# Kernel tuning notes

Hardware: AMD Instinct MI355X
Metric: run time of the kernel (lower is better)

The kernel has to match this reference:

```python
import jax, jax.numpy as jnp
import numpy as np

RESO = 32          # triplane/voxel resolution
VIT = 16           # ViT patch grid resolution
PAD = 0.1
C_TRI = 64         # triplane channels per plane
C_IMG = 1280       # image feature channels
C_IN = 128         # inner (attention) channels
C_OUT = 64
NH = 8
HD = C_IN // NH
IMG_SIZE = 224.0


def pos_enc(d_model, length):
    pos = jnp.arange(length, dtype=jnp.float32)[:, None]
    div = jnp.exp(jnp.arange(0, d_model, 2, dtype=jnp.float32) * (-np.log(10000.0) / d_model))
    pe = jnp.zeros((length, d_model), jnp.float32)
    pe = pe.at[:, 0::2].set(jnp.sin(pos * div))
    pe = pe.at[:, 1::2].set(jnp.cos(pos * div))
    return pe


def bilinear_sample(feats, gx, gy):
    # feats: [B, J, H, W, C]; gx, gy: [B, J, N] in [-1, 1]; align_corners=True
    B, J, Hh, Ww, _ = feats.shape
    ux = (gx + 1.0) * 0.5 * (Ww - 1)
    uy = (gy + 1.0) * 0.5 * (Hh - 1)
    x0 = jnp.floor(ux).astype(jnp.int32)
    y0 = jnp.floor(uy).astype(jnp.int32)
    wx = (ux - x0)[..., None]
    wy = (uy - y0)[..., None]
    x1 = jnp.clip(x0 + 1, 0, Ww - 1)
    y1 = jnp.clip(y0 + 1, 0, Hh - 1)
    x0 = jnp.clip(x0, 0, Ww - 1)
    y0 = jnp.clip(y0, 0, Hh - 1)
    bi = jnp.arange(B)[:, None, None]
    ji = jnp.arange(J)[None, :, None]
    f00 = feats[bi, ji, y0, x0]
    f01 = feats[bi, ji, y0, x1]
    f10 = feats[bi, ji, y1, x0]
    f11 = feats[bi, ji, y1, x1]
    return (f00 * (1 - wx) * (1 - wy) + f01 * wx * (1 - wy)
            + f10 * (1 - wx) * wy + f11 * wx * wy)


def forward(triplane_feat, image_feat, proj_mat, k_w, k_b, q_w, q_b, v_w, v_b,
            in_w, in_b, out_w, out_b, proj_w, proj_b):
    B, n_img = image_feat.shape[0], image_feat.shape[1]
    N = RESO ** 3
    img = image_feat[:, :, 1:, :]                        # drop CLS -> [B,J,256,C_IMG]
    image_pe = pos_enc(C_IN, VIT * VIT)[None, None]      # [1,1,256,C_IN]
    k_feat = img @ k_w.T + k_b + image_pe
    v_feat = img @ v_w.T + v_b + image_pe
    k_map = k_feat.reshape(B, n_img, VIT, VIT, C_IN)     # [B,J,H,W,C]
    v_map = v_feat.reshape(B, n_img, VIT, VIT, C_IN)

    # voxel coords -> project into each camera
    idx = jnp.arange(RESO)
    X, Y, Z = jnp.meshgrid(idx, idx, idx, indexing='ij')
    vox = jnp.stack([X, Y, Z], -1).reshape(N, 3).astype(jnp.float32)
    vox = (vox / (RESO - 1) - 0.5) * 2.0 * (1.0 + PAD + 1e-5)
    homo = jnp.concatenate([vox, jnp.ones((N, 1), jnp.float32)], -1)  # [N,4]
    pc = jnp.einsum('nk,bjik->bjni', homo, proj_mat)                   # [B,J,N,4]
    px = pc[..., 0] / pc[..., 2]
    py = pc[..., 1] / pc[..., 2]
    gx = jnp.clip((px / (IMG_SIZE - 1) - 0.5) * 2.0, -1.0, 1.0)
    gy = jnp.clip((py / (IMG_SIZE - 1) - 0.5) * 2.0, -1.0, 1.0)
    # The torch code does a 3D grid_sample whose depth coordinate lands exactly
    # on each image index (align_corners=True), so it reduces to per-image
    # bilinear sampling on the 16x16 token maps.
    k_s = bilinear_sample(k_map, gx, gy)   # [B,J,N,C_IN]
    v_s = bilinear_sample(v_map, gx, gy)

    # triplane features expanded to the voxel grid (voxel order n = x*R^2+y*R+z)
    xz, xy, yz = jnp.split(triplane_feat, 3, axis=2)     # each [B,C,R,R]
    xz_t = jnp.transpose(xz, (0, 3, 2, 1))               # [B,x,z,C]
    xy_t = jnp.transpose(xy, (0, 3, 2, 1))               # [B,x,y,C]
    yz_t = jnp.transpose(yz, (0, 3, 2, 1))               # [B,y,z,C]
    shp = (B, RESO, RESO, RESO, C_TRI)
    xz_v = jnp.broadcast_to(xz_t[:, :, None, :, :], shp)
    xy_v = jnp.broadcast_to(xy_t[:, :, :, None, :], shp)
    yz_v = jnp.broadcast_to(yz_t[:, None, :, :, :], shp)
    tri = jnp.concatenate([xz_v, xy_v, yz_v], -1).reshape(B, N, 3 * C_TRI)
    q = tri @ q_w.T + q_b + pos_enc(C_IN, N)[None]       # [B,N,C_IN]

    # per-voxel cross attention (q_len=1, kv_len=n_img); torch MHA semantics
    Wq, Wk, Wv = in_w[:C_IN], in_w[C_IN:2 * C_IN], in_w[2 * C_IN:]
    bq, bk, bv = in_b[:C_IN], in_b[C_IN:2 * C_IN], in_b[2 * C_IN:]
    qh = (q @ Wq.T + bq).reshape(B, N, NH, HD)
    k_t = jnp.transpose(k_s, (0, 2, 1, 3))               # [B,N,J,C]
    v_t = jnp.transpose(v_s, (0, 2, 1, 3))
    kh = (k_t @ Wk.T + bk).reshape(B, N, n_img, NH, HD)
    vh = (v_t @ Wv.T + bv).reshape(B, N, n_img, NH, HD)
    logits = jnp.einsum('bnhd,bnjhd->bnhj', qh, kh) / np.sqrt(HD).astype(np.float32)
    attn = jax.nn.softmax(logits, axis=-1)
    o = jnp.einsum('bnhj,bnjhd->bnhd', attn, vh).reshape(B, N, C_IN)
    o = o @ out_w.T + out_b

    # mean-pool volume back to three planes
    vol = o.reshape(B, RESO, RESO, RESO, C_IN)             # [b,x,y,z,c]
    xz_o = jnp.transpose(vol.mean(axis=2), (0, 2, 1, 3))   # [b,z,x,c]
    xy_o = jnp.transpose(vol.mean(axis=3), (0, 2, 1, 3))   # [b,y,x,c]
    yz_o = jnp.transpose(vol.mean(axis=1), (0, 2, 1, 3))   # [b,z,y,c]
    planes = jnp.concatenate([xz_o, xy_o, yz_o], axis=1)   # [B,3R,R,C_IN]
    out = planes @ proj_w.T + proj_b
    return jnp.transpose(out, (0, 3, 1, 2))                # [B,C_OUT,3R,R]


def setup_inputs() -> dict:
    key = jax.random.key(0)
    ks = jax.random.split(key, 10)
    B, J = 2, 5
    s = 0.02
    base = jnp.array([[200., 0., 112., 0.],
                      [0., 200., 112., 0.],
                      [0., 0., 1., 3.5],
                      [0., 0., 0., 1.]], jnp.float32)
    return {
        'triplane_feat': jax.random.normal(ks[0], (B, C_TRI, 3 * RESO, RESO), jnp.float32),
        'image_feat': jax.random.normal(ks[1], (B, J, VIT * VIT + 1, C_IMG), jnp.float32),
        'proj_mat': base[None, None] + 0.01 * jax.random.normal(ks[2], (B, J, 4, 4), jnp.float32),
        'valid_frames': jnp.ones((B, J), jnp.int32),
        'k_w': s * jax.random.normal(ks[3], (C_IN, C_IMG), jnp.float32), 'k_b': jnp.zeros((C_IN,), jnp.float32),
        'q_w': s * jax.random.normal(ks[4], (C_IN, 3 * C_TRI), jnp.float32), 'q_b': jnp.zeros((C_IN,), jnp.float32),
        'v_w': s * jax.random.normal(ks[5], (C_IN, C_IMG), jnp.float32), 'v_b': jnp.zeros((C_IN,), jnp.float32),
        'in_w': s * jax.random.normal(ks[6], (3 * C_IN, C_IN), jnp.float32), 'in_b': jnp.zeros((3 * C_IN,), jnp.float32),
        'out_w': s * jax.random.normal(ks[7], (C_IN, C_IN), jnp.float32), 'out_b': jnp.zeros((C_IN,), jnp.float32),
        'proj_w': s * jax.random.normal(ks[8], (C_OUT, C_IN), jnp.float32), 'proj_b': jnp.zeros((C_OUT,), jnp.float32),
    }


def reference(triplane_feat, image_feat, proj_mat, valid_frames, k_w, k_b, q_w, q_b,
              v_w, v_b, in_w, in_b, out_w, out_b, proj_w, proj_b):
    # valid_frames matches the torch forward signature but is unused in its body
    return forward(triplane_feat, image_feat, proj_mat, k_w, k_b, q_w, q_b,
                   v_w, v_b, in_w, in_b, out_w, out_b, proj_w, proj_b)
```

## Files before the change

### kernel.cpp

```cpp
#include <hip/hip_runtime.h>
#include <hip/hip_bf16.h>
#include <cstddef>

#define NVOX 32768
#define J5 5
#define KB2 1472
typedef __hip_bfloat16 bf16;
typedef __attribute__((ext_vector_type(8))) short bf16x8v;
typedef __attribute__((ext_vector_type(4))) float f32x4;

static __device__ __forceinline__ float pe_val(int pos, int c) {
  float dv = expf((float)(c & ~1) * (-0.0719557841560639f));
  float arg = (float)pos * dv;
  return (c & 1) ? cosf(arg) : sinf(arg);
}
static __device__ __forceinline__ short f2b(float f) {
  __hip_bfloat16 h = __float2bfloat16(f);
  return *reinterpret_cast<short*>(&h);
}
static __device__ __forceinline__ float b2f(short s) {
  __hip_bfloat16 h = *reinterpret_cast<__hip_bfloat16*>(&s);
  return __bfloat162float(h);
}
static __device__ __forceinline__ float2 cmul(float2 a, float2 b) {
  return make_float2(a.x * b.x - a.y * b.y, a.x * b.y + a.y * b.x);
}

#define NB_TABS   24
#define NB_WQPE   64
#define NB_WQC    96
#define NB_WO     32
#define NB_QCB    1
#define NB_TRI    1536
#define NB_FOLDW  1280
#define NB_PETAB  128
#define NB_WIN    128
#define NB_CB     1
#define B_TABS   0
#define B_WQPE   (B_TABS + NB_TABS)
#define B_WQC    (B_WQPE + NB_WQPE)
#define B_WO     (B_WQC + NB_WQC)
#define B_QCB    (B_WO + NB_WO)
#define B_TRI    (B_QCB + NB_QCB)
#define B_FOLDW  (B_TRI + NB_TRI)
#define B_PETAB  (B_FOLDW + NB_FOLDW)
#define B_WIN    (B_PETAB + NB_PETAB)
#define B_CB     (B_WIN + NB_WIN)
#define NB_TOTAL (B_CB + NB_CB)

__global__ __launch_bounds__(256) void k_prep(
    const float* __restrict__ tp,
    const float* __restrict__ k_w, const float* __restrict__ k_b,
    const float* __restrict__ q_w, const float* __restrict__ q_b,
    const float* __restrict__ v_w, const float* __restrict__ v_b,
    const float* __restrict__ in_w, const float* __restrict__ in_b,
    const float* __restrict__ out_w, const float* __restrict__ out_b,
    const float* __restrict__ proj_w, const float* __restrict__ proj_b,
    float2* __restrict__ tabs, short* __restrict__ Wqb_s, float* __restrict__ Wo,
    float* __restrict__ qcb, float* __restrict__ obb,
    short* __restrict__ tri_tb, short* __restrict__ Wkvb2, short* __restrict__ pe_tab) {
  const int bx = blockIdx.x, t = threadIdx.x;

  if (bx < B_WQPE) {
    int idx = bx * 256 + t;
    if (idx < 6144) {
      int tb = idx >> 11, rem = idx & 2047;
      int pos = rem >> 6, i = rem & 63;
      float dv = expf((float)(2 * i) * (-0.0719557841560639f));
      float mult = (tb == 0) ? 1024.0f : (tb == 1) ? 32.0f : 1.0f;
      float ang = (float)pos * mult * dv;
      tabs[idx] = make_float2(cosf(ang), sinf(ang));
    }
  } else if (bx < B_WQC) {
    int e = (bx - B_WQPE) * 256 + t;
    int c = e >> 7, j = e & 127;
    Wqb_s[(size_t)c * 320 + 192 + j] = f2b(in_w[(size_t)c * 128 + j]);
  } else if (bx < B_WO) {
    int e = (bx - B_WQC) * 256 + t;
    int c = e / 192, k = e % 192;
    const float* ir = in_w + (size_t)c * 128;
    float acc = 0.f;
    for (int j = 0; j < 128; j++) acc = fmaf(ir[j], q_w[(size_t)j * 192 + k], acc);
    Wqb_s[(size_t)c * 320 + k] = f2b(acc);
  } else if (bx < B_QCB) {
    int e = (bx - B_WO) * 256 + t;
    int o = e >> 7, c = e & 127;
    const float* pr = proj_w + (size_t)o * 128;
    float acc = 0.f;
    for (int j = 0; j < 128; j++) acc = fmaf(pr[j], out_w[(size_t)j * 128 + c], acc);
    Wo[e] = acc;
  } else if (bx < B_TRI) {
    if (t < 128) {
      float acc = in_b[t];
      const float* ir = in_w + (size_t)t * 128;
      for (int j = 0; j < 128; j++) acc = fmaf(ir[j], q_b[j], acc);
      qcb[t] = acc;
    }
    if (t < 64) {
      float acc = proj_b[t];
      const float* pr = proj_w + (size_t)t * 128;
      for (int j = 0; j < 128; j++) acc = fmaf(pr[j], out_b[j], acc);
      obb[t] = acc;
    }
  } else if (bx < B_FOLDW) {
    int idx = (bx - B_TRI) * 256 + t;
    int cc   = idx & 63;
    int rem  = idx >> 6;
    int cell = rem & 1023;
    int segb = rem >> 10;
    int seg = segb % 3, b = segb / 3;
    int i = cell >> 5, j = cell & 31;
    tri_tb[idx] = f2b(tp[(((size_t)(b * 64 + cc)) * 96 + seg * 32 + i) * 32 + j]);
  } else if (bx < B_PETAB) {
    int u = (bx - B_FOLDW) * 256 + t;
    int c = u / 1280, k = u % 1280;
    const float* w = (c < 128) ? k_w : v_w;
    const float* ir = in_w + (size_t)(128 + c) * 128;
    float acc = 0.f;
    for (int j = 0; j < 128; j++) acc = fmaf(ir[j], w[(size_t)j * 1280 + k], acc);
    Wkvb2[(size_t)c * KB2 + k] = f2b(acc);
  } else if (bx < B_WIN) {
    int e = (bx - B_PETAB) * 256 + t;
    int p = e >> 7, c = e & 127;
    pe_tab[e] = f2b(pe_val(p, c));
  } else if (bx < B_CB) {
    int e = (bx - B_WIN) * 256 + t;
    int c = e >> 7, j = e & 127;
    Wkvb2[(size_t)c * KB2 + 1280 + j] = f2b(in_w[(size_t)(128 + c) * 128 + j]);
  } else {
    int c = t;
    int which = c >> 7;
    const float* bias = which ? v_b : k_b;
    const float* ir = in_w + (size_t)(128 + c) * 128;
    float acc = in_b[128 + c];
    for (int j = 0; j < 128; j++) acc = fmaf(bias[j], ir[j], acc);
    short* row = Wkvb2 + (size_t)c * KB2 + 1408;
    row[0] = f2b(acc);
    for (int k = 1; k < 64; k++) row[k] = 0;
  }
}

__global__ __launch_bounds__(256) void k_gemm_kv(
    const float* __restrict__ img, const short* __restrict__ Wkvb2,
    const short* __restrict__ pe_tab, short* __restrict__ k2b, short* __restrict__ v2b) {
  __shared__ __align__(16) short A_lds[32 * 64];
  __shared__ __align__(16) short B_lds[64 * 64];
  const int m0 = blockIdx.x * 32;
  const int nb0 = blockIdx.y * 64;
  const int t = threadIdx.x;
  const int lane = t & 63, w = t >> 6;
  const int wm = w & 1, wn = w >> 1;
  f32x4 acc[2];
  acc[0] = (f32x4){0.f, 0.f, 0.f, 0.f};
  acc[1] = (f32x4){0.f, 0.f, 0.f, 0.f};

  for (int ct = 0; ct < 23; ct++) {
    __syncthreads();
    {
      int r = t >> 3, g = t & 7;
      bf16x8v v;
      if (ct < 20) {
        int row = m0 + r;
        int bj = row >> 8, p = row & 255;
        const float* src = img + ((size_t)(bj * 257 + 1 + p)) * 1280 + ct * 64 + g * 8;
        float4 a0 = *(const float4*)src;
        float4 a1 = *(const float4*)(src + 4);
        v[0] = f2b(a0.x); v[1] = f2b(a0.y); v[2] = f2b(a0.z); v[3] = f2b(a0.w);
        v[4] = f2b(a1.x); v[5] = f2b(a1.y); v[6] = f2b(a1.z); v[7] = f2b(a1.w);
      } else if (ct < 22) {
        int p = (m0 + r) & 255;
        v = *reinterpret_cast<const bf16x8v*>(pe_tab + (size_t)p * 128 + (ct - 20) * 64 + g * 8);
      } else {
        v = (bf16x8v){0, 0, 0, 0, 0, 0, 0, 0};
        if (g == 0) v[0] = (short)0x3F80;
      }
      *reinterpret_cast<bf16x8v*>(&A_lds[(r * 8 + (g ^ (r & 7))) * 8]) = v;
    }
    {
#pragma unroll
      for (int it = 0; it < 2; it++) {
        int u = it * 256 + t;
        int r2 = u >> 3, g = u & 7;
        const int4 src = *reinterpret_cast<const int4*>(
            Wkvb2 + (size_t)(nb0 + r2) * KB2 + ct * 64 + g * 8);
        *reinterpret_cast<int4*>(&B_lds[(r2 * 8 + (g ^ (r2 & 7))) * 8]) = src;
      }
    }
    __syncthreads();
#pragma unroll
    for (int ks = 0; ks < 2; ks++) {
      int kb = ks * 4 + (lane >> 4);
      int arow = wm * 16 + (lane & 15);
      bf16x8v a = *reinterpret_cast<const bf16x8v*>(&A_lds[(arow * 8 + (kb ^ (arow & 7))) * 8]);
#pragma unroll
      for (int f = 0; f < 2; f++) {
        int bcol = wn * 32 + f * 16 + (lane & 15);
        bf16x8v bb = *reinterpret_cast<const bf16x8v*>(&B_lds[(bcol * 8 + (kb ^ (bcol & 7))) * 8]);
        acc[f] = __builtin_amdgcn_mfma_f32_16x16x32_bf16(a, bb, acc[f], 0, 0, 0);
      }
    }
  }
#pragma unroll
  for (int f = 0; f < 2; f++) {
#pragma unroll
    for (int reg = 0; reg < 4; reg++) {
      int grow = m0 + wm * 16 + (lane >> 4) * 4 + reg;
      int gcol = nb0 + wn * 32 + f * 16 + (lane & 15);
      int which = gcol >> 7, c = gcol & 127;
      short* dst = which ? v2b : k2b;
      dst[(size_t)grow * 128 + c] = f2b(acc[f][reg]);
    }
  }
}

__global__ __launch_bounds__(256) void k_qh(
    const short* __restrict__ tri_tb, const short* __restrict__ Wqb_s,
    const float* __restrict__ qcb, const float2* __restrict__ tabs,
    short* __restrict__ qh_g) {
  __shared__ __align__(16) short A_lds[64 * 64];
  __shared__ __align__(16) short B_lds[128 * 64];
  const int b = blockIdx.y;
  const int n0 = blockIdx.x * 64;
  const int t = threadIdx.x;
  const int lane = t & 63, w = t >> 6;
  const int xq = n0 >> 10, yq0 = (n0 >> 5) & 31;
  const float2* tabX = tabs;
  const float2* tabY = tabs + 2048;
  const float2* tabZ = tabs + 4096;

  f32x4 acc[4][2];
#pragma unroll
  for (int m = 0; m < 4; m++)
#pragma unroll
    for (int f = 0; f < 2; f++) acc[m][f] = (f32x4){0.f, 0.f, 0.f, 0.f};

  for (int ct = 0; ct < 5; ct++) {
    __syncthreads();
    {
#pragma unroll
      for (int it = 0; it < 2; it++) {
        int u = it * 256 + t;
        int r = u >> 3, g = u & 7;
        if (ct < 3) {
          int n = n0 + r;
          int x = n >> 10, y = (n >> 5) & 31, z = n & 31;
          int cell = (ct == 0) ? (z * 32 + x) : (ct == 1) ? (y * 32 + x) : (z * 32 + y);
          const int4 src = *reinterpret_cast<const int4*>(
              tri_tb + ((size_t)(b * 3 + ct) * 1024 + cell) * 64 + g * 8);
          *reinterpret_cast<int4*>(&A_lds[(r * 8 + (g ^ (r & 7))) * 8]) = src;
        } else {
          int i0 = (ct - 3) * 32 + g * 4;
          int z = r & 31, y = yq0 + (r >> 5);
          bf16x8v v;
#pragma unroll
          for (int q = 0; q < 4; q++) {
            int i = i0 + q;
            float2 exy = cmul(tabX[xq * 64 + i], tabY[y * 64 + i]);
            float2 e = cmul(exy, tabZ[z * 64 + i]);
            v[q * 2]     = f2b(e.y);
            v[q * 2 + 1] = f2b(e.x);
          }
          *reinterpret_cast<bf16x8v*>(&A_lds[(r * 8 + (g ^ (r & 7))) * 8]) = v;
        }
      }
    }
    {
#pragma unroll
      for (int it = 0; it < 4; it++) {
        int u = it * 256 + t;
        int col = u >> 3, g = u & 7;
        const int4 src = *reinterpret_cast<const int4*>(
            Wqb_s + (size_t)col * 320 + ct * 64 + g * 8);
        *reinterpret_cast<int4*>(&B_lds[(col * 8 + (g ^ (col & 7))) * 8]) = src;
      }
    }
    __syncthreads();
#pragma unroll
    for (int ks = 0; ks < 2; ks++) {
      int kb = ks * 4 + (lane >> 4);
      bf16x8v a[4], bb[2];
#pragma unroll
      for (int m = 0; m < 4; m++) {
        int row = m * 16 + (lane & 15);
        a[m] = *reinterpret_cast<const bf16x8v*>(&A_lds[(row * 8 + (kb ^ (row & 7))) * 8]);
      }
#pragma unroll
      for (int f = 0; f < 2; f++) {
        int col = w * 32 + f * 16 + (lane & 15);
        bb[f] = *reinterpret_cast<const bf16x8v*>(&B_lds[(col * 8 + (kb ^ (col & 7))) * 8]);
      }
#pragma unroll
      for (int m = 0; m < 4; m++)
#pragma unroll
        for (int f = 0; f < 2; f++)
          acc[m][f] = __builtin_amdgcn_mfma_f32_16x16x32_bf16(a[m], bb[f], acc[m][f], 0, 0, 0);
    }
  }
#pragma unroll
  for (int m = 0; m < 4; m++)
#pragma unroll
    for (int f = 0; f < 2; f++)
#pragma unroll
      for (int reg = 0; reg < 4; reg++) {
        int row = m * 16 + (lane >> 4) * 4 + reg;
        int col = w * 32 + f * 16 + (lane & 15);
        qh_g[((size_t)b * NVOX + n0 + row) * 128 + col] = f2b(acc[m][f][reg] + qcb[col]);
      }
}

__global__ __launch_bounds__(256) void k_attn(
    const short* __restrict__ qh_g, const short* __restrict__ k2b,
    const short* __restrict__ v2b, const float* __restrict__ proj,
    bf16* __restrict__ obuf) {
  __shared__ __align__(16) ushort sIr[160][4];
  __shared__ __align__(16) float sW4[160][4];
  __shared__ __align__(16) float lg[160 * 8];
  const int b = blockIdx.y;
  const int n0 = blockIdx.x * 32;
  const int t = threadIdx.x;

  if (t < 160) {
    int r = t / J5, j = t % J5;
    int n = n0 + r;
    int x = n >> 10, y = (n >> 5) & 31, z = n & 31;
    const float SC = (float)(1.0 + 0.1 + 1e-05);
    float fx = ((float)x / 31.0f - 0.5f) * 2.0f * SC;
    float fy = ((float)y / 31.0f - 0.5f) * 2.0f * SC;
    float fz = ((float)z / 31.0f - 0.5f) * 2.0f * SC;
    const float* P = proj + (size_t)(b * J5 + j) * 16;
    float pc0 = fmaf(fx, P[0], fmaf(fy, P[1], fmaf(fz, P[2],  P[3])));
    float pc1 = fmaf(fx, P[4], fmaf(fy, P[5], fmaf(fz, P[6],  P[7])));
    float pc2 = fmaf(fx, P[8], fmaf(fy, P[9], fmaf(fz, P[10], P[11])));
    float px = pc0 / pc2, py = pc1 / pc2;
    float gx = fminf(fmaxf((px / 223.0f - 0.5f) * 2.0f, -1.0f), 1.0f);
    float gy = fminf(fmaxf((py / 223.0f - 0.5f) * 2.0f, -1.0f), 1.0f);
    float ux = (gx + 1.0f) * 0.5f * 15.0f;
    float uy = (gy + 1.0f) * 0.5f * 15.0f;
    float fx0 = floorf(ux), fy0 = floorf(uy);
    int x0 = (int)fx0, y0 = (int)fy0;
    float wx = ux - fx0, wy = uy - fy0;
    int x1 = min(x0 + 1, 15), y1 = min(y0 + 1, 15);
    x0 = min(max(x0, 0), 15); y0 = min(max(y0, 0), 15);
    int rowb = (b * J5 + j) * 256;
    sIr[t][0] = (ushort)(rowb + y0 * 16 + x0);
    sIr[t][1] = (ushort)(rowb + y0 * 16 + x1);
    sIr[t][2] = (ushort)(rowb + y1 * 16 + x0);
    sIr[t][3] = (ushort)(rowb + y1 * 16 + x1);
    sW4[t][0] = (1.f - wx) * (1.f - wy);
    sW4[t][1] = wx * (1.f - wy);
    sW4[t][2] = (1.f - wx) * wy;
    sW4[t][3] = wx * wy;
  }
  __syncthreads();

  {
    const int oct = t & 15, rjIdx = t >> 4;
    const int c0 = oct * 8;
#pragma unroll
    for (int it = 0; it < 10; it++) {
      int rj = rjIdx + it * 16;
      int r = rj / J5;
      ushort4 I4 = *reinterpret_cast<const ushort4*>(sIr[rj]);
      float4 W4 = *reinterpret_cast<const float4*>(sW4[rj]);
      bf16x8v t0 = *reinterpret_cast<const bf16x8v*>(k2b + (size_t)I4.x * 128 + c0);
      bf16x8v t1 = *reinterpret_cast<const bf16x8v*>(k2b + (size_t)I4.y * 128 + c0);
      bf16x8v t2 = *reinterpret_cast<const bf16x8v*>(k2b + (size_t)I4.z * 128 + c0);
      bf16x8v t3 = *reinterpret_cast<const bf16x8v*>(k2b + (size_t)I4.w * 128 + c0);
      bf16x8v q8 = *reinterpret_cast<const bf16x8v*>(qh_g + ((size_t)b * NVOX + n0 + r) * 128 + c0);
      float pv = 0.f;
#pragma unroll
      for (int e = 0; e < 8; e++) {
        float kh = fmaf(W4.x, b2f(t0[e]), fmaf(W4.y, b2f(t1[e]),
                   fmaf(W4.z, b2f(t2[e]), W4.w * b2f(t3[e]))));
        pv = fmaf(b2f(q8[e]), kh, pv);
      }
      pv += __shfl_xor(pv, 1);
      if (!(oct & 1)) lg[rj * 8 + (oct >> 1)] = pv * 0.25f;
    }
  }
  __syncthreads();

  {
    int r = t >> 3, h = t & 7;
    float l[J5];
    float m = -1e30f;
#pragma unroll
    for (int j = 0; j < J5; j++) { l[j] = lg[(r * J5 + j) * 8 + h]; m = fmaxf(m, l[j]); }
    float sden = 0.f;
#pragma unroll
    for (int j = 0; j < J5; j++) { l[j] = expf(l[j] - m); sden += l[j]; }
    float inv = 1.0f / sden;
#pragma unroll
    for (int j = 0; j < J5; j++) lg[(r * J5 + j) * 8 + h] = l[j] * inv;
  }
  __syncthreads();

  {
    const int oct = t & 15;
    const int c0 = oct * 8;
#pragma unroll
    for (int it = 0; it < 2; it++) {
      int r = (t >> 4) + it * 16;
      float o8[8] = {0.f, 0.f, 0.f, 0.f, 0.f, 0.f, 0.f, 0.f};
#pragma unroll
      for (int j = 0; j < J5; j++) {
        int rj = r * J5 + j;
        float aw = lg[rj * 8 + (oct >> 1)];
        ushort4 I4 = *reinterpret_cast<const ushort4*>(sIr[rj]);
        float4 W4 = *reinterpret_cast<const float4*>(sW4[rj]);
        float w0 = aw * W4.x, w1 = aw * W4.y, w2 = aw * W4.z, w3 = aw * W4.w;
        bf16x8v t0 = *reinterpret_cast<const bf16x8v*>(v2b + (size_t)I4.x * 128 + c0);
        bf16x8v t1 = *reinterpret_cast<const bf16x8v*>(v2b + (size_t)I4.y * 128 + c0);
        bf16x8v t2 = *reinterpret_cast<const bf16x8v*>(v2b + (size_t)I4.z * 128 + c0);
        bf16x8v t3 = *reinterpret_cast<const bf16x8v*>(v2b + (size_t)I4.w * 128 + c0);
#pragma unroll
        for (int e = 0; e < 8; e++) {
          o8[e] = fmaf(w0, b2f(t0[e]), o8[e]);
          o8[e] = fmaf(w1, b2f(t1[e]), o8[e]);
          o8[e] = fmaf(w2, b2f(t2[e]), o8[e]);
          o8[e] = fmaf(w3, b2f(t3[e]), o8[e]);
        }
      }
      bf16x8v out;
#pragma unroll
      for (int e = 0; e < 8; e++) out[e] = f2b(o8[e]);
      *reinterpret_cast<bf16x8v*>((short*)obuf + ((size_t)b * NVOX + n0 + r) * 128 + c0) = out;
    }
  }
}

__global__ __launch_bounds__(128) void k_reduce(const bf16* __restrict__ obuf,
                                                float* __restrict__ pacc) {
  int blk = blockIdx.x;
  int b = blockIdx.y;
  int t = threadIdx.x;
  int oct = t & 15, sub = t >> 4;
  int c0 = oct * 8;
  int cell = blk * 8 + sub;
  const short* ob = (const short*)obuf + (size_t)b * NVOX * 128;
  float a8[8] = {0.f, 0.f, 0.f, 0.f, 0.f, 0.f, 0.f, 0.f};
  size_t prow;
  if (cell < 1024) {
    int z = cell >> 5, x = cell & 31;
    for (int y = 0; y < 32; y++) {
      bf16x8v u = *reinterpret_cast<const bf16x8v*>(ob + ((size_t)(x * 1024 + y * 32 + z) * 128 + c0));
#pragma unroll
      for (int e = 0; e < 8; e++) a8[e] += b2f(u[e]);
    }
    prow = ((size_t)(b * 96 + z) * 32 + x) * 128 + c0;
  } else if (cell < 2048) {
    int e2 = cell - 1024;
    int y = e2 >> 5, x = e2 & 31;
    for (int z = 0; z < 32; z++) {
      bf16x8v u = *reinterpret_cast<const bf16x8v*>(ob + ((size_t)(x * 1024 + y * 32 + z) * 128 + c0));
#pragma unroll
      for (int e = 0; e < 8; e++) a8[e] += b2f(u[e]);
    }
    prow = ((size_t)(b * 96 + 32 + y) * 32 + x) * 128 + c0;
  } else {
    int e2 = cell - 2048;
    int z = e2 >> 5, y = e2 & 31;
    for (int x = 0; x < 32; x++) {
      bf16x8v u = *reinterpret_cast<const bf16x8v*>(ob + ((size_t)(x * 1024 + y * 32 + z) * 128 + c0));
#pragma unroll
      for (int e = 0; e < 8; e++) a8[e] += b2f(u[e]);
    }
    prow = ((size_t)(b * 96 + 64 + z) * 32 + y) * 128 + c0;
  }
  *(float4*)(&pacc[prow])     = (float4){a8[0], a8[1], a8[2], a8[3]};
  *(float4*)(&pacc[prow + 4]) = (float4){a8[4], a8[5], a8[6], a8[7]};
}

__global__ __launch_bounds__(128) void k_final(
    const float* __restrict__ pacc, const float* __restrict__ Wo,
    const float* __restrict__ obb, float* __restrict__ outp) {
  int bp = blockIdx.x;
  int b = bp / 96, prow = bp % 96;
  int obase = blockIdx.y * 16;
  __shared__ __align__(16) float lds[32 * 129];
  for (int idx = threadIdx.x; idx < 4096; idx += 128) {
    int col = idx >> 7, k = idx & 127;
    lds[col * 129 + k] = pacc[(size_t)bp * 32 * 128 + idx] * (1.0f / 32.0f);
  }
  __syncthreads();
  for (int e = threadIdx.x; e < 16 * 32; e += 128) {
    int o = obase + (e >> 5), col = e & 31;
    float val = obb[o];
    const float* wr = Wo + (size_t)o * 128;
    const float* lr = lds + col * 129;
    for (int k = 0; k < 128; k++) val = fmaf(wr[k], lr[k], val);
    outp[((size_t)(b * 64 + o) * 96 + prow) * 32 + col] = val;
  }
}

extern "C" void kernel_launch(void* const* d_in, const int* in_sizes, int n_in,
                              void* d_out, int out_size, void* d_ws, size_t ws_size,
                              hipStream_t stream) {
  const float* tp     = (const float*)d_in[0];
  const float* img    = (const float*)d_in[1];
  const float* proj   = (const float*)d_in[2];
  const float* k_w    = (const float*)d_in[4];
  const float* k_b    = (const float*)d_in[5];
  const float* q_w    = (const float*)d_in[6];
  const float* q_b    = (const float*)d_in[7];
  const float* v_w    = (const float*)d_in[8];
  const float* v_b    = (const float*)d_in[9];
  const float* in_w   = (const float*)d_in[10];
  const float* in_b   = (const float*)d_in[11];
  const float* out_w  = (const float*)d_in[12];
  const float* out_b  = (const float*)d_in[13];
  const float* proj_w = (const float*)d_in[14];
  const float* proj_b = (const float*)d_in[15];
  const int B = 2;

  float* ws = (float*)d_ws;
  size_t off = 0;
  short*  tri_tb = (short*)(ws + off);  off += 196608;
  short*  Wkvb2  = (short*)(ws + off);  off += 188416;
  short*  Wqb_s  = (short*)(ws + off);  off += 20480;
  short*  pe_tab = (short*)(ws + off);  off += 16384;
  float2* tabs   = (float2*)(ws + off); off += 12288;
  float*  qcb    = ws + off;            off += 128;
  float*  Wo     = ws + off;            off += 8192;
  float*  obb    = ws + off;            off += 64;
  short*  k2b    = (short*)(ws + off);  off += 163840;
  short*  v2b    = (short*)(ws + off);  off += 163840;
  float*  pacc   = ws + off;            off += 786432;
  short*  qh_g   = (short*)(ws + off);  off += 4194304;
  bf16*   obuf   = (bf16*)(ws + off);   off += 2097152;
  if (ws_size < off * sizeof(float)) return;

  k_prep<<<dim3(NB_TOTAL), dim3(256), 0, stream>>>(
      tp, k_w, k_b, q_w, q_b, v_w, v_b, in_w, in_b, out_w, out_b, proj_w, proj_b,
      tabs, Wqb_s, Wo, qcb, obb, tri_tb, Wkvb2, pe_tab);
  k_gemm_kv<<<dim3(80, 4), dim3(256), 0, stream>>>(img, Wkvb2, pe_tab, k2b, v2b);
  k_qh<<<dim3(NVOX / 64, B), dim3(256), 0, stream>>>(tri_tb, Wqb_s, qcb, tabs, qh_g);
  k_attn<<<dim3(NVOX / 32, B), dim3(256), 0, stream>>>(qh_g, k2b, v2b, proj, obuf);
  k_reduce<<<dim3(384, B), dim3(128), 0, stream>>>(obuf, pacc);
  k_final<<<dim3(B * 96, 4), dim3(128), 0, stream>>>(pacc, Wo, obb, (float*)d_out);
}
```

Baseline: 110.5 us.

## Merge KV and Q GEMMs into one launch, fuse xy-plane reduction into attention

The K/V projection GEMM and the Q-head GEMM now run as one kernel launch, with blocks split by blockIdx, which removes a launch and lets the two independent GEMMs overlap. The attention kernel also sums its 32 contiguous-z voxels per (x,y) directly from LDS into the xy-plane accumulator, so the reduce kernel only handles the other two planes. The triplane transpose in prep now goes through an LDS tile with vectorized loads and stores instead of scattered per-element writes. The cost is extra LDS and a block-wide barrier in attention, plus a mixed-role kernel whose blocks have uneven work.

```diff
diff --git a/kernel.cpp b/kernel.cpp
--- a/kernel.cpp
+++ b/kernel.cpp
@@ -31,7 +31,7 @@
 #define NB_WQC    96
 #define NB_WO     32
 #define NB_QCB    1
-#define NB_TRI    1536
+#define NB_TRI2   96
 #define NB_FOLDW  1280
 #define NB_PETAB  128
 #define NB_WIN    128
@@ -41,8 +41,8 @@
 #define B_WQC    (B_WQPE + NB_WQPE)
 #define B_WO     (B_WQC + NB_WQC)
 #define B_QCB    (B_WO + NB_WO)
-#define B_TRI    (B_QCB + NB_QCB)
-#define B_FOLDW  (B_TRI + NB_TRI)
+#define B_TRI2   (B_QCB + NB_QCB)
+#define B_FOLDW  (B_TRI2 + NB_TRI2)
 #define B_PETAB  (B_FOLDW + NB_FOLDW)
 #define B_WIN    (B_PETAB + NB_PETAB)
 #define B_CB     (B_WIN + NB_WIN)
@@ -59,6 +59,7 @@
     float2* __restrict__ tabs, short* __restrict__ Wqb_s, float* __restrict__ Wo,
     float* __restrict__ qcb, float* __restrict__ obb,
     short* __restrict__ tri_tb, short* __restrict__ Wkvb2, short* __restrict__ pe_tab) {
+  __shared__ short tile_s[64][65];
   const int bx = blockIdx.x, t = threadIdx.x;
 
   if (bx < B_WQPE) {
@@ -89,7 +90,7 @@
     float acc = 0.f;
     for (int j = 0; j < 128; j++) acc = fmaf(pr[j], out_w[(size_t)j * 128 + c], acc);
     Wo[e] = acc;
-  } else if (bx < B_TRI) {
+  } else if (bx < B_TRI2) {
     if (t < 128) {
       float acc = in_b[t];
       const float* ir = in_w + (size_t)t * 128;
@@ -103,14 +104,29 @@
       obb[t] = acc;
     }
   } else if (bx < B_FOLDW) {
-    int idx = (bx - B_TRI) * 256 + t;
-    int cc   = idx & 63;
-    int rem  = idx >> 6;
-    int cell = rem & 1023;
-    int segb = rem >> 10;
-    int seg = segb % 3, b = segb / 3;
-    int i = cell >> 5, j = cell & 31;
-    tri_tb[idx] = f2b(tp[(((size_t)(b * 64 + cc)) * 96 + seg * 32 + i) * 32 + j]);
+    int b3 = bx - B_TRI2;
+    int segb = b3 >> 4, tile = b3 & 15;
+    int b = segb / 3, seg = segb % 3;
+    int cc = t >> 2, q = t & 3;
+#pragma unroll
+    for (int di = 0; di < 2; di++) {
+      int i = tile * 2 + di;
+      const float* src = tp + (((size_t)(b * 64 + cc)) * 96 + seg * 32 + i) * 32 + q * 8;
+      float4 a0 = *(const float4*)src;
+      float4 a1 = *(const float4*)(src + 4);
+      short* dst = &tile_s[cc][di * 32 + q * 8];
+      dst[0] = f2b(a0.x); dst[1] = f2b(a0.y); dst[2] = f2b(a0.z); dst[3] = f2b(a0.w);
+      dst[4] = f2b(a1.x); dst[5] = f2b(a1.y); dst[6] = f2b(a1.z); dst[7] = f2b(a1.w);
+    }
+    __syncthreads();
+    int cp = t >> 2;
+    int cc0 = q * 16;
+    bf16x8v v0, v1;
+#pragma unroll
+    for (int e = 0; e < 8; e++) { v0[e] = tile_s[cc0 + e][cp]; v1[e] = tile_s[cc0 + 8 + e][cp]; }
+    short* outp = tri_tb + (((size_t)(b * 3 + seg) * 1024) + tile * 64 + cp) * 64 + cc0;
+    *reinterpret_cast<bf16x8v*>(outp) = v0;
+    *reinterpret_cast<bf16x8v*>(outp + 8) = v1;
   } else if (bx < B_PETAB) {
     int u = (bx - B_FOLDW) * 256 + t;
     int c = u / 1280, k = u % 1280;
@@ -140,181 +156,181 @@
   }
 }
 
-__global__ __launch_bounds__(256) void k_gemm_kv(
+#define NKV 320
+__global__ __launch_bounds__(256) void k_qkv(
     const float* __restrict__ img, const short* __restrict__ Wkvb2,
-    const short* __restrict__ pe_tab, short* __restrict__ k2b, short* __restrict__ v2b) {
-  __shared__ __align__(16) short A_lds[32 * 64];
-  __shared__ __align__(16) short B_lds[64 * 64];
-  const int m0 = blockIdx.x * 32;
-  const int nb0 = blockIdx.y * 64;
-  const int t = threadIdx.x;
-  const int lane = t & 63, w = t >> 6;
-  const int wm = w & 1, wn = w >> 1;
-  f32x4 acc[2];
-  acc[0] = (f32x4){0.f, 0.f, 0.f, 0.f};
-  acc[1] = (f32x4){0.f, 0.f, 0.f, 0.f};
-
-  for (int ct = 0; ct < 23; ct++) {
-    __syncthreads();
-    {
-      int r = t >> 3, g = t & 7;
-      bf16x8v v;
-      if (ct < 20) {
-        int row = m0 + r;
-        int bj = row >> 8, p = row & 255;
-        const float* src = img + ((size_t)(bj * 257 + 1 + p)) * 1280 + ct * 64 + g * 8;
-        float4 a0 = *(const float4*)src;
-        float4 a1 = *(const float4*)(src + 4);
-        v[0] = f2b(a0.x); v[1] = f2b(a0.y); v[2] = f2b(a0.z); v[3] = f2b(a0.w);
-        v[4] = f2b(a1.x); v[5] = f2b(a1.y); v[6] = f2b(a1.z); v[7] = f2b(a1.w);
-      } else if (ct < 22) {
-        int p = (m0 + r) & 255;
-        v = *reinterpret_cast<const bf16x8v*>(pe_tab + (size_t)p * 128 + (ct - 20) * 64 + g * 8);
-      } else {
-        v = (bf16x8v){0, 0, 0, 0, 0, 0, 0, 0};
-        if (g == 0) v[0] = (short)0x3F80;
-      }
-      *reinterpret_cast<bf16x8v*>(&A_lds[(r * 8 + (g ^ (r & 7))) * 8]) = v;
-    }
-    {
-#pragma unroll
-      for (int it = 0; it < 2; it++) {
-        int u = it * 256 + t;
-        int r2 = u >> 3, g = u & 7;
-        const int4 src = *reinterpret_cast<const int4*>(
-            Wkvb2 + (size_t)(nb0 + r2) * KB2 + ct * 64 + g * 8);
-        *reinterpret_cast<int4*>(&B_lds[(r2 * 8 + (g ^ (r2 & 7))) * 8]) = src;
-      }
-    }
-    __syncthreads();
-#pragma unroll
-    for (int ks = 0; ks < 2; ks++) {
-      int kb = ks * 4 + (lane >> 4);
-      int arow = wm * 16 + (lane & 15);
-      bf16x8v a = *reinterpret_cast<const bf16x8v*>(&A_lds[(arow * 8 + (kb ^ (arow & 7))) * 8]);
-#pragma unroll
-      for (int f = 0; f < 2; f++) {
-        int bcol = wn * 32 + f * 16 + (lane & 15);
-        bf16x8v bb = *reinterpret_cast<const bf16x8v*>(&B_lds[(bcol * 8 + (kb ^ (bcol & 7))) * 8]);
-        acc[f] = __builtin_amdgcn_mfma_f32_16x16x32_bf16(a, bb, acc[f], 0, 0, 0);
-      }
-    }
-  }
-#pragma unroll
-  for (int f = 0; f < 2; f++) {
-#pragma unroll
-    for (int reg = 0; reg < 4; reg++) {
-      int grow = m0 + wm * 16 + (lane >> 4) * 4 + reg;
-      int gcol = nb0 + wn * 32 + f * 16 + (lane & 15);
-      int which = gcol >> 7, c = gcol & 127;
-      short* dst = which ? v2b : k2b;
-      dst[(size_t)grow * 128 + c] = f2b(acc[f][reg]);
-    }
-  }
-}
-
-__global__ __launch_bounds__(256) void k_qh(
+    const short* __restrict__ pe_tab, short* __restrict__ k2b, short* __restrict__ v2b,
     const short* __restrict__ tri_tb, const short* __restrict__ Wqb_s,
     const float* __restrict__ qcb, const float2* __restrict__ tabs,
     short* __restrict__ qh_g) {
   __shared__ __align__(16) short A_lds[64 * 64];
   __shared__ __align__(16) short B_lds[128 * 64];
-  const int b = blockIdx.y;
-  const int n0 = blockIdx.x * 64;
   const int t = threadIdx.x;
   const int lane = t & 63, w = t >> 6;
-  const int xq = n0 >> 10, yq0 = (n0 >> 5) & 31;
-  const float2* tabX = tabs;
-  const float2* tabY = tabs + 2048;
-  const float2* tabZ = tabs + 4096;
-
-  f32x4 acc[4][2];
-#pragma unroll
-  for (int m = 0; m < 4; m++)
-#pragma unroll
-    for (int f = 0; f < 2; f++) acc[m][f] = (f32x4){0.f, 0.f, 0.f, 0.f};
-
-  for (int ct = 0; ct < 5; ct++) {
-    __syncthreads();
-    {
-#pragma unroll
-      for (int it = 0; it < 2; it++) {
-        int u = it * 256 + t;
-        int r = u >> 3, g = u & 7;
-        if (ct < 3) {
-          int n = n0 + r;
-          int x = n >> 10, y = (n >> 5) & 31, z = n & 31;
-          int cell = (ct == 0) ? (z * 32 + x) : (ct == 1) ? (y * 32 + x) : (z * 32 + y);
+
+  if (blockIdx.x < NKV) {
+    const int kvid = blockIdx.x;
+    const int m0 = (kvid >> 2) * 32;
+    const int nb0 = (kvid & 3) * 64;
+    const int wm = w & 1, wn = w >> 1;
+    f32x4 acc[2];
+    acc[0] = (f32x4){0.f, 0.f, 0.f, 0.f};
+    acc[1] = (f32x4){0.f, 0.f, 0.f, 0.f};
+    for (int ct = 0; ct < 23; ct++) {
+      __syncthreads();
+      {
+        int r = t >> 3, g = t & 7;
+        bf16x8v v;
+        if (ct < 20) {
+          int row = m0 + r;
+          int bj = row >> 8, p = row & 255;
+          const float* src = img + ((size_t)(bj * 257 + 1 + p)) * 1280 + ct * 64 + g * 8;
+          float4 a0 = *(const float4*)src;
+          float4 a1 = *(const float4*)(src + 4);
+          v[0] = f2b(a0.x); v[1] = f2b(a0.y); v[2] = f2b(a0.z); v[3] = f2b(a0.w);
+          v[4] = f2b(a1.x); v[5] = f2b(a1.y); v[6] = f2b(a1.z); v[7] = f2b(a1.w);
+        } else if (ct < 22) {
+          int p = (m0 + r) & 255;
+          v = *reinterpret_cast<const bf16x8v*>(pe_tab + (size_t)p * 128 + (ct - 20) * 64 + g * 8);
+        } else {
+          v = (bf16x8v){0, 0, 0, 0, 0, 0, 0, 0};
+          if (g == 0) v[0] = (short)0x3F80;
+        }
+        *reinterpret_cast<bf16x8v*>(&A_lds[(r * 8 + (g ^ (r & 7))) * 8]) = v;
+      }
+      {
+#pragma unroll
+        for (int it = 0; it < 2; it++) {
+          int u = it * 256 + t;
+          int r2 = u >> 3, g = u & 7;
           const int4 src = *reinterpret_cast<const int4*>(
-              tri_tb + ((size_t)(b * 3 + ct) * 1024 + cell) * 64 + g * 8);
-          *reinterpret_cast<int4*>(&A_lds[(r * 8 + (g ^ (r & 7))) * 8]) = src;
-        } else {
-          int i0 = (ct - 3) * 32 + g * 4;
-          int z = r & 31, y = yq0 + (r >> 5);
-          bf16x8v v;
-#pragma unroll
-          for (int q = 0; q < 4; q++) {
-            int i = i0 + q;
-            float2 exy = cmul(tabX[xq * 64 + i], tabY[y * 64 + i]);
-            float2 e = cmul(exy, tabZ[z * 64 + i]);
-            v[q * 2]     = f2b(e.y);
-            v[q * 2 + 1] = f2b(e.x);
+              Wkvb2 + (size_t)((kvid & 3) * 64 + r2) * KB2 + ct * 64 + g * 8);
+          *reinterpret_cast<int4*>(&B_lds[(r2 * 8 + (g ^ (r2 & 7))) * 8]) = src;
+        }
+      }
+      __syncthreads();
+#pragma unroll
+      for (int ks = 0; ks < 2; ks++) {
+        int kb = ks * 4 + (lane >> 4);
+        int arow = wm * 16 + (lane & 15);
+        bf16x8v a = *reinterpret_cast<const bf16x8v*>(&A_lds[(arow * 8 + (kb ^ (arow & 7))) * 8]);
+#pragma unroll
+        for (int f = 0; f < 2; f++) {
+          int bcol = wn * 32 + f * 16 + (lane & 15);
+          bf16x8v bb = *reinterpret_cast<const bf16x8v*>(&B_lds[(bcol * 8 + (kb ^ (bcol & 7))) * 8]);
+          acc[f] = __builtin_amdgcn_mfma_f32_16x16x32_bf16(a, bb, acc[f], 0, 0, 0);
+        }
+      }
+    }
+#pragma unroll
+    for (int f = 0; f < 2; f++) {
+#pragma unroll
+      for (int reg = 0; reg < 4; reg++) {
+        int grow = m0 + wm * 16 + (lane >> 4) * 4 + reg;
+        int gcol = nb0 + wn * 32 + f * 16 + (lane & 15);
+        int which = gcol >> 7, c = gcol & 127;
+        short* dst = which ? v2b : k2b;
+        dst[(size_t)grow * 128 + c] = f2b(acc[f][reg]);
+      }
+    }
+  } else {
+    const int qid = blockIdx.x - NKV;
+    const int b = qid >> 9;
+    const int n0 = (qid & 511) * 64;
+    const int xq = n0 >> 10, yq0 = (n0 >> 5) & 31;
+    const float2* tabX = tabs;
+    const float2* tabY = tabs + 2048;
+    const float2* tabZ = tabs + 4096;
+    f32x4 acc[4][2];
+#pragma unroll
+    for (int m = 0; m < 4; m++)
+#pragma unroll
+      for (int f = 0; f < 2; f++) acc[m][f] = (f32x4){0.f, 0.f, 0.f, 0.f};
+
+    for (int ct = 0; ct < 5; ct++) {
+      __syncthreads();
+      {
+#pragma unroll
+        for (int it = 0; it < 2; it++) {
+          int u = it * 256 + t;
+          int r = u >> 3, g = u & 7;
+          if (ct < 3) {
+            int n = n0 + r;
+            int x = n >> 10, y = (n >> 5) & 31, z = n & 31;
+            int cell = (ct == 0) ? (z * 32 + x) : (ct == 1) ? (y * 32 + x) : (z * 32 + y);
+            const int4 src = *reinterpret_cast<const int4*>(
+                tri_tb + ((size_t)(b * 3 + ct) * 1024 + cell) * 64 + g * 8);
+            *reinterpret_cast<int4*>(&A_lds[(r * 8 + (g ^ (r & 7))) * 8]) = src;
+          } else {
+            int i0 = (ct - 3) * 32 + g * 4;
+            int z = r & 31, y = yq0 + (r >> 5);
+            bf16x8v v;
+#pragma unroll
+            for (int q = 0; q < 4; q++) {
+              int i = i0 + q;
+              float2 exy = cmul(tabX[xq * 64 + i], tabY[y * 64 + i]);
+              float2 e = cmul(exy, tabZ[z * 64 + i]);
+              v[q * 2]     = f2b(e.y);
+              v[q * 2 + 1] = f2b(e.x);
+            }
+            *reinterpret_cast<bf16x8v*>(&A_lds[(r * 8 + (g ^ (r & 7))) * 8]) = v;
           }
-          *reinterpret_cast<bf16x8v*>(&A_lds[(r * 8 + (g ^ (r & 7))) * 8]) = v;
-        }
-      }
-    }
-    {
-#pragma unroll
-      for (int it = 0; it < 4; it++) {
-        int u = it * 256 + t;
-        int col = u >> 3, g = u & 7;
-        const int4 src = *reinterpret_cast<const int4*>(
-            Wqb_s + (size_t)col * 320 + ct * 64 + g * 8);
-        *reinterpret_cast<int4*>(&B_lds[(col * 8 + (g ^ (col & 7))) * 8]) = src;
-      }
-    }
-    __syncthreads();
-#pragma unroll
-    for (int ks = 0; ks < 2; ks++) {
-      int kb = ks * 4 + (lane >> 4);
-      bf16x8v a[4], bb[2];
-#pragma unroll
-      for (int m = 0; m < 4; m++) {
-        int row = m * 16 + (lane & 15);
-        a[m] = *reinterpret_cast<const bf16x8v*>(&A_lds[(row * 8 + (kb ^ (row & 7))) * 8]);
-      }
-#pragma unroll
-      for (int f = 0; f < 2; f++) {
-        int col = w * 32 + f * 16 + (lane & 15);
-        bb[f] = *reinterpret_cast<const bf16x8v*>(&B_lds[(col * 8 + (kb ^ (col & 7))) * 8]);
-      }
-#pragma unroll
-      for (int m = 0; m < 4; m++)
-#pragma unroll
-        for (int f = 0; f < 2; f++)
-          acc[m][f] = __builtin_amdgcn_mfma_f32_16x16x32_bf16(a[m], bb[f], acc[m][f], 0, 0, 0);
-    }
-  }
-#pragma unroll
-  for (int m = 0; m < 4; m++)
-#pragma unroll
-    for (int f = 0; f < 2; f++)
-#pragma unroll
-      for (int reg = 0; reg < 4; reg++) {
-        int row = m * 16 + (lane >> 4) * 4 + reg;
-        int col = w * 32 + f * 16 + (lane & 15);
-        qh_g[((size_t)b * NVOX + n0 + row) * 128 + col] = f2b(acc[m][f][reg] + qcb[col]);
-      }
+        }
+      }
+      {
+#pragma unroll
+        for (int it = 0; it < 4; it++) {
+          int u = it * 256 + t;
+          int col = u >> 3, g = u & 7;
+          const int4 src = *reinterpret_cast<const int4*>(
+              Wqb_s + (size_t)col * 320 + ct * 64 + g * 8);
+          *reinterpret_cast<int4*>(&B_lds[(col * 8 + (g ^ (col & 7))) * 8]) = src;
+        }
+      }
+      __syncthreads();
+#pragma unroll
+      for (int ks = 0; ks < 2; ks++) {
+        int kb = ks * 4 + (lane >> 4);
+        bf16x8v a[4], bb[2];
+#pragma unroll
+        for (int m = 0; m < 4; m++) {
+          int row = m * 16 + (lane & 15);
+          a[m] = *reinterpret_cast<const bf16x8v*>(&A_lds[(row * 8 + (kb ^ (row & 7))) * 8]);
+        }
+#pragma unroll
+        for (int f = 0; f < 2; f++) {
+          int col = w * 32 + f * 16 + (lane & 15);
+          bb[f] = *reinterpret_cast<const bf16x8v*>(&B_lds[(col * 8 + (kb ^ (col & 7))) * 8]);
+        }
+#pragma unroll
+        for (int m = 0; m < 4; m++)
+#pragma unroll
+          for (int f = 0; f < 2; f++)
+            acc[m][f] = __builtin_amdgcn_mfma_f32_16x16x32_bf16(a[m], bb[f], acc[m][f], 0, 0, 0);
+      }
+    }
+#pragma unroll
+    for (int m = 0; m < 4; m++)
+#pragma unroll
+      for (int f = 0; f < 2; f++)
+#pragma unroll
+        for (int reg = 0; reg < 4; reg++) {
+          int row = m * 16 + (lane >> 4) * 4 + reg;
+          int col = w * 32 + f * 16 + (lane & 15);
+          qh_g[((size_t)b * NVOX + n0 + row) * 128 + col] = f2b(acc[m][f][reg] + qcb[col]);
+        }
+  }
 }
 
 __global__ __launch_bounds__(256) void k_attn(
     const short* __restrict__ qh_g, const short* __restrict__ k2b,
     const short* __restrict__ v2b, const float* __restrict__ proj,
-    bf16* __restrict__ obuf) {
+    bf16* __restrict__ obuf, float* __restrict__ pacc) {
   __shared__ __align__(16) ushort sIr[160][4];
   __shared__ __align__(16) float sW4[160][4];
   __shared__ __align__(16) float lg[160 * 8];
+  __shared__ __align__(16) short o_lds[32][128];
+  __shared__ float sxy[2][128];
   const int b = blockIdx.y;
   const int n0 = blockIdx.x * 32;
   const int t = threadIdx.x;
@@ -425,7 +441,22 @@
 #pragma unroll
       for (int e = 0; e < 8; e++) out[e] = f2b(o8[e]);
       *reinterpret_cast<bf16x8v*>((short*)obuf + ((size_t)b * NVOX + n0 + r) * 128 + c0) = out;
-    }
+      *reinterpret_cast<bf16x8v*>(&o_lds[r][c0]) = out;
+    }
+  }
+  __syncthreads();
+
+  {
+    int c = t & 127, half = t >> 7;
+    float s = 0.f;
+#pragma unroll
+    for (int i = 0; i < 16; i++) s += b2f(o_lds[half * 16 + i][c]);
+    sxy[half][c] = s;
+  }
+  __syncthreads();
+  if (t < 128) {
+    int x = n0 >> 10, y = (n0 >> 5) & 31;
+    pacc[((size_t)(b * 96 + 32 + y) * 32 + x) * 128 + t] = sxy[0][t] + sxy[1][t];
   }
 }
 
@@ -448,17 +479,8 @@
       for (int e = 0; e < 8; e++) a8[e] += b2f(u[e]);
     }
     prow = ((size_t)(b * 96 + z) * 32 + x) * 128 + c0;
-  } else if (cell < 2048) {
+  } else {
     int e2 = cell - 1024;
-    int y = e2 >> 5, x = e2 & 31;
-    for (int z = 0; z < 32; z++) {
-      bf16x8v u = *reinterpret_cast<const bf16x8v*>(ob + ((size_t)(x * 1024 + y * 32 + z) * 128 + c0));
-#pragma unroll
-      for (int e = 0; e < 8; e++) a8[e] += b2f(u[e]);
-    }
-    prow = ((size_t)(b * 96 + 32 + y) * 32 + x) * 128 + c0;
-  } else {
-    int e2 = cell - 2048;
     int z = e2 >> 5, y = e2 & 31;
     for (int x = 0; x < 32; x++) {
       bf16x8v u = *reinterpret_cast<const bf16x8v*>(ob + ((size_t)(x * 1024 + y * 32 + z) * 128 + c0));
@@ -533,9 +555,9 @@
   k_prep<<<dim3(NB_TOTAL), dim3(256), 0, stream>>>(
       tp, k_w, k_b, q_w, q_b, v_w, v_b, in_w, in_b, out_w, out_b, proj_w, proj_b,
       tabs, Wqb_s, Wo, qcb, obb, tri_tb, Wkvb2, pe_tab);
-  k_gemm_kv<<<dim3(80, 4), dim3(256), 0, stream>>>(img, Wkvb2, pe_tab, k2b, v2b);
-  k_qh<<<dim3(NVOX / 64, B), dim3(256), 0, stream>>>(tri_tb, Wqb_s, qcb, tabs, qh_g);
-  k_attn<<<dim3(NVOX / 32, B), dim3(256), 0, stream>>>(qh_g, k2b, v2b, proj, obuf);
-  k_reduce<<<dim3(384, B), dim3(128), 0, stream>>>(obuf, pacc);
+  k_qkv<<<dim3(NKV + NVOX / 64 * B), dim3(256), 0, stream>>>(
+      img, Wkvb2, pe_tab, k2b, v2b, tri_tb, Wqb_s, qcb, tabs, qh_g);
+  k_attn<<<dim3(NVOX / 32, B), dim3(256), 0, stream>>>(qh_g, k2b, v2b, proj, obuf, pacc);
+  k_reduce<<<dim3(256, B), dim3(128), 0, stream>>>(obuf, pacc);
   k_final<<<dim3(B * 96, 4), dim3(128), 0, stream>>>(pacc, Wo, obb, (float*)d_out);
 }
```

Result: faster. 95.54 us (-13.5%).
